# Kernel tuning notes

Hardware: AMD Instinct MI355X
Metric: run time of the kernel (lower is better)

## Reference

```python
import jax, jax.numpy as jnp
import numpy as np

N_SUP, N_SUB, LATENT, OUT = 256, 1024, 512, 200


def list_of_distances(X, Y):
    # squared Euclidean pairwise distances: (len(X), len(Y))
    xx = jnp.sum(X * X, axis=1, keepdims=True)          # (n, 1)
    yy = jnp.sum(Y * Y, axis=1)[None, :]                # (1, m)
    return xx - 2.0 * (X @ Y.T) + yy


def setup_inputs() -> dict:
    key = jax.random.key(0)
    ks = jax.random.split(key, 7)
    x = jax.random.normal(ks[0], (32768, LATENT), dtype=jnp.float32)
    sup_prototypes = jax.random.uniform(ks[1], (N_SUP, LATENT), dtype=jnp.float32)
    sub_prototypes = jax.random.uniform(ks[2], (N_SUB, LATENT), dtype=jnp.float32)
    lim1 = 1.0 / np.sqrt(N_SUP)
    lim2 = 1.0 / np.sqrt(N_SUB)
    W1 = jax.random.uniform(ks[3], (OUT, N_SUP), dtype=jnp.float32, minval=-lim1, maxval=lim1)
    b1 = jax.random.uniform(ks[4], (OUT,), dtype=jnp.float32, minval=-lim1, maxval=lim1)
    W2 = jax.random.uniform(ks[5], (OUT, N_SUB), dtype=jnp.float32, minval=-lim2, maxval=lim2)
    b2 = jax.random.uniform(ks[6], (OUT,), dtype=jnp.float32, minval=-lim2, maxval=lim2)
    return {"x": x, "sup_prototypes": sup_prototypes, "sub_prototypes": sub_prototypes,
            "W1": W1, "b1": b1, "W2": W2, "b2": b2}


def reference(x, sup_prototypes, sub_prototypes, W1, b1, W2, b2):
    sup_input_dist = list_of_distances(x, sup_prototypes)   # (B, n_sup)
    sub_input_dist = list_of_distances(x, sub_prototypes)   # (B, n_sub)
    sup_out = sup_input_dist @ W1.T + b1                     # (B, out)
    sub_out = sub_input_dist @ W2.T + b2                     # (B, out)
    sub_clones = jax.lax.stop_gradient(sub_prototypes)
    super_sub_dist = list_of_distances(sup_prototypes, sub_clones)  # (n_sup, n_sub)
    r1 = jnp.mean(jnp.min(sub_input_dist, axis=0))
    r2 = jnp.mean(jnp.min(sub_input_dist, axis=1))
    r3 = jnp.mean(jnp.min(super_sub_dist, axis=1))
    r4 = jnp.mean(jnp.min(super_sub_dist, axis=0))
    return (sub_out, sup_out, r1, r2, r3, r4)
```

## Files before the change

kernel.cpp:

```cpp
#include <hip/hip_runtime.h>
#include <stdint.h>

#define BATCH   32768
#define NSUP    256
#define NSUB    1024
#define LATENT  512
#define NOUT    200
#define SUP_OFF ((size_t)BATCH * NOUT)

typedef unsigned short u16;
typedef __attribute__((ext_vector_type(8))) __bf16 bf16x8;
typedef __attribute__((ext_vector_type(4))) float  floatx4;

typedef const __attribute__((address_space(1))) void* gptr_t;
typedef __attribute__((address_space(3))) void* sptr_t;

__device__ __forceinline__ void gload16(const void* g, void* l) {
  __builtin_amdgcn_global_load_lds((gptr_t)g, (sptr_t)l, 16, 0, 0);
}

__device__ __forceinline__ floatx4 mfma_bf16(bf16x8 a, bf16x8 b, floatx4 c) {
  return __builtin_amdgcn_mfma_f32_16x16x32_bf16(a, b, c, 0, 0, 0);
}

__device__ __forceinline__ u16 f2bf(float f) {
  unsigned int u = __float_as_uint(f);
  u += 0x7FFFu + ((u >> 16) & 1u);
  return (u16)(u >> 16);
}

__device__ __forceinline__ size_t bfoff(int c, int k) {
  return (size_t)(c >> 4) * 8192 + (size_t)((k >> 5) * 512)
       + (size_t)((((k >> 3) & 3) * 16 + (c & 15)) * 8) + (size_t)(k & 7);
}

__global__ __launch_bounds__(256) void k_setup(const float* __restrict__ sup,
    const float* __restrict__ sub, const float* __restrict__ W1,
    const float* __restrict__ W2, u16* __restrict__ sups, u16* __restrict__ subs,
    u16* __restrict__ Bf, float* __restrict__ MtF, float* __restrict__ xxsup,
    float* __restrict__ yys, unsigned int* __restrict__ minbuf,
    float* __restrict__ out4) {
  __shared__ float lw[8 * 256];
  int bx = blockIdx.x;
  if (bx >= 458) {
    int idx = bx - 458;
    if (idx >= 400) {
      int z = idx - 400;
      int k = (z & 1) * 256 + threadIdx.x;
      int o0 = 400 + (z >> 1) * 8;
      for (int oo = 0; oo < 8; oo++) Bf[bfoff(o0 + oo, k)] = 0;
      return;
    }
    int jc = idx & 3;
    int kb = (idx >> 2) & 1;
    int o0 = (idx >> 3) * 8;
    int k  = kb * 256 + threadIdx.x;
    const float* P; const float* W; int n, ow;
    if (o0 < 200) { P = sup; W = W1; n = NSUP;  ow = o0; }
    else          { P = sub; W = W2; n = NSUB;  ow = o0 - 200; }
    int nq = n >> 2;
    int j0 = jc * nq;
    for (int i = threadIdx.x; i < 8 * nq; i += 256) {
      int oo = i / nq, j = i - oo * nq;
      lw[oo * 256 + j] = W[(size_t)(ow + oo) * n + j0 + j];
    }
    __syncthreads();
    float a[8] = {};
    for (int j = 0; j < nq; j += 8) {
      float pv[8];
#pragma unroll
      for (int u = 0; u < 8; u++) pv[u] = P[(size_t)(j0 + j + u) * LATENT + k];
#pragma unroll
      for (int oo = 0; oo < 8; oo++) {
        float acc = 0.f;
#pragma unroll
        for (int u = 0; u < 8; u++) acc += pv[u] * lw[oo * 256 + j + u];
        a[oo] += acc;
      }
    }
#pragma unroll
    for (int oo = 0; oo < 8; oo++)
      MtF[((size_t)jc * 400 + o0 + oo) * 512 + k] = a[oo];
    return;
  }
  if (bx >= 320) {
    if (bx == 457) { if (threadIdx.x < 4) out4[threadIdx.x] = 0.f; return; }
    int i = (bx - 320) * 256 + threadIdx.x;
    if (i < BATCH + NSUP + 2 * NSUB) minbuf[i] = 0x7F800000u;
    return;
  }
  int row  = bx * 4 + (threadIdx.x >> 6);
  int lane = threadIdx.x & 63;
  const float* src; u16* dst; float* nrm; int subrow = -1;
  if (row < NSUP) { src = sup + (size_t)row * LATENT; dst = sups + (size_t)row * LATENT; nrm = xxsup + row; }
  else { int r = row - NSUP; subrow = r; src = sub + (size_t)r * LATENT; dst = subs + (size_t)r * LATENT; nrm = yys + r; }
  const float* s = src + lane * 8;
  float4 v0 = ((const float4*)s)[0];
  float4 v1 = ((const float4*)s)[1];
  float ss = v0.x*v0.x + v0.y*v0.y + v0.z*v0.z + v0.w*v0.w
           + v1.x*v1.x + v1.y*v1.y + v1.z*v1.z + v1.w*v1.w;
  uint4 o;
  o.x = (unsigned)f2bf(v0.x) | ((unsigned)f2bf(v0.y) << 16);
  o.y = (unsigned)f2bf(v0.z) | ((unsigned)f2bf(v0.w) << 16);
  o.z = (unsigned)f2bf(v1.x) | ((unsigned)f2bf(v1.y) << 16);
  o.w = (unsigned)f2bf(v1.z) | ((unsigned)f2bf(v1.w) << 16);
  *((uint4*)(dst + lane * 8)) = o;
  if (subrow >= 0) {
    size_t off = (size_t)(32 + (subrow >> 4)) * 8192 + (size_t)((lane >> 2) * 512)
               + (size_t)((((lane & 3) * 16) + (subrow & 15)) * 8);
    *((uint4*)(Bf + off)) = o;
  }
  for (int off = 32; off; off >>= 1) ss += __shfl_down(ss, off);
  if (lane == 0) *nrm = ss;
}

__global__ __launch_bounds__(256) void k_scc(const float* __restrict__ W1,
    const float* __restrict__ b1, const float* __restrict__ W2,
    const float* __restrict__ b2, const float* __restrict__ xxsup,
    const float* __restrict__ yys, float* __restrict__ sc, float* __restrict__ cc,
    const u16* __restrict__ sups, const u16* __restrict__ subs,
    const float* __restrict__ MtF, u16* __restrict__ Bf,
    unsigned int* __restrict__ rowmin, unsigned int* __restrict__ colsup) {
  __shared__ __align__(16) u16 lA[128 * 64];
  __shared__ __align__(16) u16 lB[128 * 64];
  int bx = blockIdx.x;
  if (bx >= 116) {
    int o = bx - 116;
    for (int k = threadIdx.x; k < 512; k += 256) {
      float s = MtF[((size_t)0 * 400 + o) * 512 + k]
              + MtF[((size_t)1 * 400 + o) * 512 + k]
              + MtF[((size_t)2 * 400 + o) * 512 + k]
              + MtF[((size_t)3 * 400 + o) * 512 + k];
      Bf[bfoff(o, k)] = f2bf(-2.f * s);
    }
    return;
  }
  if (bx >= 100) {
    int bid = bx - 100;
    int cb = bid & 7;
    size_t arow0 = (size_t)(bid >> 3) * 128;
    const u16* B = subs + (size_t)cb * 128 * LATENT;
    floatx4 acc[4][4] = {};
    int t = threadIdx.x, wave = t >> 6, lane = t & 63;
    int l16 = lane & 15, qq = lane >> 4;
    int wm = (wave >> 1) * 64, wn = (wave & 1) * 64;
    int sq = (lane & 7) ^ (lane >> 3);
    const u16* Ab = sups + arow0 * LATENT;
    int soff[4]; u16 *dA[4], *dB[4];
#pragma unroll
    for (int i = 0; i < 4; i++) {
      int s = i * 256 + t;
      soff[i] = (s >> 3) * LATENT + sq * 8;
      int sbase = (i * 256 + wave * 64) * 8;
      dA[i] = lA + sbase; dB[i] = lB + sbase;
    }
    for (int k0 = 0; k0 < LATENT; k0 += 64) {
#pragma unroll
      for (int i = 0; i < 4; i++) gload16(Ab + soff[i] + k0, dA[i]);
#pragma unroll
      for (int i = 0; i < 4; i++) gload16(B  + soff[i] + k0, dB[i]);
      __syncthreads();
#pragma unroll
      for (int ks = 0; ks < 2; ks++) {
        bf16x8 af[4], bvv[4];
        int sw = ((ks * 4 + qq) ^ (l16 & 7)) * 8;
#pragma unroll
        for (int f = 0; f < 4; f++) {
          af[f]  = *(const bf16x8*)(lA + (wm + f * 16 + l16) * 64 + sw);
          bvv[f] = *(const bf16x8*)(lB + (wn + f * 16 + l16) * 64 + sw);
        }
#pragma unroll
        for (int fm = 0; fm < 4; fm++)
#pragma unroll
          for (int fn = 0; fn < 4; fn++)
            acc[fm][fn] = mfma_bf16(af[fm], bvv[fn], acc[fm][fn]);
      }
      __syncthreads();
    }
    int colb = cb * 128 + wn + l16;
    float yv[4];
#pragma unroll
    for (int fn = 0; fn < 4; fn++) yv[fn] = yys[colb + fn * 16];
    float cmin[4] = {3.4e38f, 3.4e38f, 3.4e38f, 3.4e38f};
#pragma unroll
    for (int fm = 0; fm < 4; fm++) {
#pragma unroll
      for (int r = 0; r < 4; r++) {
        int row = (int)arow0 + wm + fm * 16 + qq * 4 + r;
        float xvv = xxsup[row];
        float rmin = 3.4e38f;
#pragma unroll
        for (int fn = 0; fn < 4; fn++) {
          float d = xvv - 2.0f * acc[fm][fn][r] + yv[fn];
          rmin = fminf(rmin, d);
          cmin[fn] = fminf(cmin[fn], d);
        }
        for (int off = 1; off < 16; off <<= 1) rmin = fminf(rmin, __shfl_xor(rmin, off));
        if (l16 == 0) atomicMin(rowmin + BATCH + row, __float_as_uint(rmin));
      }
    }
#pragma unroll
    for (int fn = 0; fn < 4; fn++) {
      float v = cmin[fn];
      v = fminf(v, __shfl_xor(v, 16));
      v = fminf(v, __shfl_xor(v, 32));
      if (qq == 0) atomicMin(colsup + colb + fn * 16, __float_as_uint(v));
    }
    return;
  }
  int wave = threadIdx.x >> 6, lane = threadIdx.x & 63;
  int o = bx * 4 + wave;
  if (o >= 400) return;
  int n; const float* Wr; const float* yy;
  if (o < 200) { n = NSUP; Wr = W1 + (size_t)o * NSUP; yy = xxsup; }
  else         { n = NSUB; Wr = W2 + (size_t)(o - 200) * NSUB; yy = yys; }
  float s = 0.f, c = 0.f;
  for (int j = lane; j < n; j += 64) { float w = Wr[j]; s += w; c += w * yy[j]; }
  for (int off = 32; off; off >>= 1) { s += __shfl_down(s, off); c += __shfl_down(c, off); }
  if (lane == 0) { sc[o] = s; cc[o] = c + ((o < 200) ? b1[o] : b2[o - 200]); }
}

__global__ __launch_bounds__(512, 2) void k_gemm_x(const float* __restrict__ x,
    const u16* __restrict__ Bf, const float* __restrict__ yys,
    const float* __restrict__ sc, const float* __restrict__ cc,
    float* __restrict__ out, unsigned int* __restrict__ rowmin,
    unsigned int* __restrict__ colx) {
  __shared__ __align__(16) u16 lA[128 * 512];
  __shared__ float lxx[128];
  int t = threadIdx.x, wave = t >> 6, lane = t & 63;
  int l16 = lane & 15, qq = lane >> 4;
  int wr = wave >> 2, wc = wave & 3;
  size_t arow0 = (size_t)blockIdx.x * 128;

  const float* Ab = x + arow0 * LATENT;
#pragma unroll
  for (int i = 0; i < 16; i++) {
    int row = i * 8 + wave;
    const float* s = Ab + (size_t)row * LATENT + lane * 8;
    float4 v0 = ((const float4*)s)[0];
    float4 v1 = ((const float4*)s)[1];
    float ss = v0.x*v0.x + v0.y*v0.y + v0.z*v0.z + v0.w*v0.w
             + v1.x*v1.x + v1.y*v1.y + v1.z*v1.z + v1.w*v1.w;
    uint4 o;
    o.x = (unsigned)f2bf(v0.x) | ((unsigned)f2bf(v0.y) << 16);
    o.y = (unsigned)f2bf(v0.z) | ((unsigned)f2bf(v0.w) << 16);
    o.z = (unsigned)f2bf(v1.x) | ((unsigned)f2bf(v1.y) << 16);
    o.w = (unsigned)f2bf(v1.z) | ((unsigned)f2bf(v1.w) << 16);
    *((uint4*)(lA + ((row * 64) + (lane ^ (row & 7))) * 8)) = o;
    for (int off = 32; off; off >>= 1) ss += __shfl_down(ss, off);
    if (lane == 0) lxx[row] = ss;
  }
  __syncthreads();

  float xv[4][4];
#pragma unroll
  for (int mf = 0; mf < 4; mf++)
#pragma unroll
    for (int r = 0; r < 4; r++) xv[mf][r] = lxx[wr * 64 + mf * 16 + qq * 4 + r];
  float rmreg[4][4];
#pragma unroll
  for (int mf = 0; mf < 4; mf++)
#pragma unroll
    for (int r = 0; r < 4; r++) rmreg[mf][r] = 3.4e38f;

#pragma unroll 1
  for (int p = 0; p < 6; p++) {
    floatx4 acc[4][4] = {};
    const u16* Bw = Bf + (size_t)(p * 16 + wc * 4) * 8192 + lane * 8;
#pragma unroll 2
    for (int k0 = 0; k0 < LATENT; k0 += 64) {
      bf16x8 bv[4][2];
#pragma unroll
      for (int nf = 0; nf < 4; nf++)
#pragma unroll
        for (int ks = 0; ks < 2; ks++)
          bv[nf][ks] = *(const bf16x8*)(Bw + nf * 8192 + k0 * 16 + ks * 512);
#pragma unroll
      for (int ks = 0; ks < 2; ks++) {
        bf16x8 a[4];
#pragma unroll
        for (int mf = 0; mf < 4; mf++) {
          int row = wr * 64 + mf * 16 + l16;
          int kc = (k0 >> 3) + ks * 4 + qq;
          a[mf] = *(const bf16x8*)(lA + ((row * 64) + (kc ^ (row & 7))) * 8);
        }
#pragma unroll
        for (int mf = 0; mf < 4; mf++)
#pragma unroll
          for (int nf = 0; nf < 4; nf++)
            acc[mf][nf] = mfma_bf16(a[mf], bv[nf][ks], acc[mf][nf]);
      }
    }
    if (p < 2) {
      int colbase = p * 256 + wc * 64;
#pragma unroll
      for (int nf = 0; nf < 4; nf++) {
        int c = colbase + nf * 16 + l16;
        if (c < 400) {
          float scv = sc[c], ccv = cc[c];
#pragma unroll
          for (int mf = 0; mf < 4; mf++)
#pragma unroll
            for (int r = 0; r < 4; r++) {
              size_t row = arow0 + wr * 64 + mf * 16 + qq * 4 + r;
              float v = acc[mf][nf][r] + xv[mf][r] * scv + ccv;
              size_t idx = (c < 200) ? (SUP_OFF + row * NOUT + c)
                                     : (row * NOUT + (c - 200));
              out[idx] = v;
            }
        }
      }
    } else {
      int colbase = p * 256 + wc * 64 - 512;
#pragma unroll
      for (int nf = 0; nf < 4; nf++) {
        int cs = colbase + nf * 16 + l16;
        float yv = yys[cs];
        float cmin = 3.4e38f;
#pragma unroll
        for (int mf = 0; mf < 4; mf++)
#pragma unroll
          for (int r = 0; r < 4; r++) {
            float d = xv[mf][r] - 2.0f * acc[mf][nf][r] + yv;
            rmreg[mf][r] = fminf(rmreg[mf][r], d);
            cmin = fminf(cmin, d);
          }
        cmin = fminf(cmin, __shfl_xor(cmin, 16));
        cmin = fminf(cmin, __shfl_xor(cmin, 32));
        if (qq == 0) atomicMin(colx + cs, __float_as_uint(cmin));
      }
    }
  }
#pragma unroll
  for (int mf = 0; mf < 4; mf++)
#pragma unroll
    for (int r = 0; r < 4; r++) {
      float v = rmreg[mf][r];
      v = fminf(v, __shfl_xor(v, 1));
      v = fminf(v, __shfl_xor(v, 2));
      v = fminf(v, __shfl_xor(v, 4));
      v = fminf(v, __shfl_xor(v, 8));
      if (l16 == 0)
        atomicMin(rowmin + arow0 + wr * 64 + mf * 16 + qq * 4 + r, __float_as_uint(v));
    }
}

__global__ __launch_bounds__(256) void k_final2(const unsigned int* __restrict__ rowmin,
    const unsigned int* __restrict__ colx, const unsigned int* __restrict__ colsup,
    float* __restrict__ out4) {
  int bx = blockIdx.x, t = threadIdx.x;
  const unsigned int* src; int n; float scale; int slot;
  if (bx < 32)      { src = rowmin + bx * 1024; n = 1024; scale = 1.f / BATCH; slot = 1; }
  else if (bx == 32){ src = colx;               n = 1024; scale = 1.f / NSUB;  slot = 0; }
  else if (bx == 33){ src = rowmin + BATCH;     n = 256;  scale = 1.f / NSUP;  slot = 2; }
  else              { src = colsup;             n = 1024; scale = 1.f / NSUB;  slot = 3; }
  float s = 0.f;
  for (int i = t; i < n; i += 256) s += __uint_as_float(src[i]);
  __shared__ float red[4];
  for (int off = 32; off; off >>= 1) s += __shfl_down(s, off);
  if ((t & 63) == 0) red[t >> 6] = s;
  __syncthreads();
  if (t == 0) atomicAdd(out4 + slot, (red[0] + red[1] + red[2] + red[3]) * scale);
}

extern "C" void kernel_launch(void* const* d_in, const int* in_sizes, int n_in,
                              void* d_out, int out_size, void* d_ws, size_t ws_size,
                              hipStream_t stream) {
  const float* x   = (const float*)d_in[0];
  const float* sup = (const float*)d_in[1];
  const float* sub = (const float*)d_in[2];
  const float* W1  = (const float*)d_in[3];
  const float* b1  = (const float*)d_in[4];
  const float* W2  = (const float*)d_in[5];
  const float* b2  = (const float*)d_in[6];
  float* out = (float*)d_out;

  char* p = (char*)d_ws;
  u16* Bf    = (u16*)p;            p += (size_t)(512 + NSUB) * LATENT * 2;
  u16* subs  = (u16*)p;            p += (size_t)NSUB * LATENT * 2;
  u16* sups  = (u16*)p;            p += (size_t)NSUP * LATENT * 2;
  float* xxsup = (float*)p;        p += NSUP * 4;
  float* yys   = (float*)p;        p += NSUB * 4;
  float* sc    = (float*)p;        p += 512 * 4;
  float* cc    = (float*)p;        p += 512 * 4;
  unsigned int* rowmin = (unsigned int*)p; p += (size_t)(BATCH + NSUP) * 4;
  unsigned int* colx   = (unsigned int*)p; p += (size_t)NSUB * 4;
  unsigned int* colsup = (unsigned int*)p; p += (size_t)NSUB * 4;
  float* MtF   = (float*)p;        p += (size_t)4 * 400 * 512 * 4;

  float* out4 = out + 2 * SUP_OFF;

  hipLaunchKernelGGL(k_setup, dim3(886), dim3(256), 0, stream,
                     sup, sub, W1, W2, sups, subs, Bf, MtF, xxsup, yys, rowmin, out4);
  hipLaunchKernelGGL(k_scc, dim3(516), dim3(256), 0, stream,
                     W1, b1, W2, b2, xxsup, yys, sc, cc, sups, subs, MtF, Bf,
                     rowmin, colsup);
  hipLaunchKernelGGL(k_gemm_x, dim3(BATCH / 128), dim3(512), 0, stream,
                     x, Bf, yys, sc, cc, out, rowmin, colx);
  hipLaunchKernelGGL(k_final2, dim3(35), dim3(256), 0, stream, rowmin, colx, colsup, out4);
}
```

Before: 118.6 us.

## Shrink gemm row tile to 64 and spread eight waves across columns

The main GEMM kernel now processes 64 rows per block instead of 128, with all eight waves splitting the columns (512 per pass, 3 passes) rather than a 2x4 row/column wave grid over 6 passes. LDS use is halved and launch bounds raised to 4 blocks per CU, aiming for more occupancy and more blocks across the device. Row-min reduction now happens per pass with extra atomics, and each B fragment is reused across fewer A rows, so global/L2 traffic for B per output increases.

```diff
diff --git a/kernel.cpp b/kernel.cpp
--- a/kernel.cpp
+++ b/kernel.cpp
@@ -220,21 +220,21 @@
   if (lane == 0) { sc[o] = s; cc[o] = c + ((o < 200) ? b1[o] : b2[o - 200]); }
 }
 
-__global__ __launch_bounds__(512, 2) void k_gemm_x(const float* __restrict__ x,
+__global__ __launch_bounds__(512, 4) void k_gemm_x(const float* __restrict__ x,
     const u16* __restrict__ Bf, const float* __restrict__ yys,
     const float* __restrict__ sc, const float* __restrict__ cc,
     float* __restrict__ out, unsigned int* __restrict__ rowmin,
     unsigned int* __restrict__ colx) {
-  __shared__ __align__(16) u16 lA[128 * 512];
-  __shared__ float lxx[128];
+  __shared__ __align__(16) u16 lA[64 * 512];
+  __shared__ float lxx[64];
   int t = threadIdx.x, wave = t >> 6, lane = t & 63;
   int l16 = lane & 15, qq = lane >> 4;
-  int wr = wave >> 2, wc = wave & 3;
-  size_t arow0 = (size_t)blockIdx.x * 128;
+  int wc = wave;
+  size_t arow0 = (size_t)blockIdx.x * 64;
 
   const float* Ab = x + arow0 * LATENT;
 #pragma unroll
-  for (int i = 0; i < 16; i++) {
+  for (int i = 0; i < 8; i++) {
     int row = i * 8 + wave;
     const float* s = Ab + (size_t)row * LATENT + lane * 8;
     float4 v0 = ((const float4*)s)[0];
@@ -252,21 +252,10 @@
   }
   __syncthreads();
 
-  float xv[4][4];
-#pragma unroll
-  for (int mf = 0; mf < 4; mf++)
-#pragma unroll
-    for (int r = 0; r < 4; r++) xv[mf][r] = lxx[wr * 64 + mf * 16 + qq * 4 + r];
-  float rmreg[4][4];
-#pragma unroll
-  for (int mf = 0; mf < 4; mf++)
-#pragma unroll
-    for (int r = 0; r < 4; r++) rmreg[mf][r] = 3.4e38f;
-
 #pragma unroll 1
-  for (int p = 0; p < 6; p++) {
+  for (int p = 0; p < 3; p++) {
     floatx4 acc[4][4] = {};
-    const u16* Bw = Bf + (size_t)(p * 16 + wc * 4) * 8192 + lane * 8;
+    const u16* Bw = Bf + (size_t)(p * 32 + wc * 4) * 8192 + lane * 8;
 #pragma unroll 2
     for (int k0 = 0; k0 < LATENT; k0 += 64) {
       bf16x8 bv[4][2];
@@ -280,7 +269,7 @@
         bf16x8 a[4];
 #pragma unroll
         for (int mf = 0; mf < 4; mf++) {
-          int row = wr * 64 + mf * 16 + l16;
+          int row = mf * 16 + l16;
           int kc = (k0 >> 3) + ks * 4 + qq;
           a[mf] = *(const bf16x8*)(lA + ((row * 64) + (kc ^ (row & 7))) * 8);
         }
@@ -291,8 +280,13 @@
             acc[mf][nf] = mfma_bf16(a[mf], bv[nf][ks], acc[mf][nf]);
       }
     }
-    if (p < 2) {
-      int colbase = p * 256 + wc * 64;
+    float xr[4][4];
+#pragma unroll
+    for (int mf = 0; mf < 4; mf++)
+#pragma unroll
+      for (int r = 0; r < 4; r++) xr[mf][r] = lxx[mf * 16 + qq * 4 + r];
+    if (p == 0) {
+      int colbase = wc * 64;
 #pragma unroll
       for (int nf = 0; nf < 4; nf++) {
         int c = colbase + nf * 16 + l16;
@@ -302,8 +296,8 @@
           for (int mf = 0; mf < 4; mf++)
 #pragma unroll
             for (int r = 0; r < 4; r++) {
-              size_t row = arow0 + wr * 64 + mf * 16 + qq * 4 + r;
-              float v = acc[mf][nf][r] + xv[mf][r] * scv + ccv;
+              size_t row = arow0 + mf * 16 + qq * 4 + r;
+              float v = acc[mf][nf][r] + xr[mf][r] * scv + ccv;
               size_t idx = (c < 200) ? (SUP_OFF + row * NOUT + c)
                                      : (row * NOUT + (c - 200));
               out[idx] = v;
@@ -311,7 +305,12 @@
         }
       }
     } else {
-      int colbase = p * 256 + wc * 64 - 512;
+      int colbase = (p - 1) * 512 + wc * 64;
+      float rm[4][4];
+#pragma unroll
+      for (int mf = 0; mf < 4; mf++)
+#pragma unroll
+        for (int r = 0; r < 4; r++) rm[mf][r] = 3.4e38f;
 #pragma unroll
       for (int nf = 0; nf < 4; nf++) {
         int cs = colbase + nf * 16 + l16;
@@ -321,28 +320,28 @@
         for (int mf = 0; mf < 4; mf++)
 #pragma unroll
           for (int r = 0; r < 4; r++) {
-            float d = xv[mf][r] - 2.0f * acc[mf][nf][r] + yv;
-            rmreg[mf][r] = fminf(rmreg[mf][r], d);
+            float d = xr[mf][r] - 2.0f * acc[mf][nf][r] + yv;
+            rm[mf][r] = fminf(rm[mf][r], d);
             cmin = fminf(cmin, d);
           }
         cmin = fminf(cmin, __shfl_xor(cmin, 16));
         cmin = fminf(cmin, __shfl_xor(cmin, 32));
         if (qq == 0) atomicMin(colx + cs, __float_as_uint(cmin));
       }
-    }
-  }
-#pragma unroll
-  for (int mf = 0; mf < 4; mf++)
-#pragma unroll
-    for (int r = 0; r < 4; r++) {
-      float v = rmreg[mf][r];
-      v = fminf(v, __shfl_xor(v, 1));
-      v = fminf(v, __shfl_xor(v, 2));
-      v = fminf(v, __shfl_xor(v, 4));
-      v = fminf(v, __shfl_xor(v, 8));
-      if (l16 == 0)
-        atomicMin(rowmin + arow0 + wr * 64 + mf * 16 + qq * 4 + r, __float_as_uint(v));
-    }
+#pragma unroll
+      for (int mf = 0; mf < 4; mf++)
+#pragma unroll
+        for (int r = 0; r < 4; r++) {
+          float v = rm[mf][r];
+          v = fminf(v, __shfl_xor(v, 1));
+          v = fminf(v, __shfl_xor(v, 2));
+          v = fminf(v, __shfl_xor(v, 4));
+          v = fminf(v, __shfl_xor(v, 8));
+          if (l16 == 0)
+            atomicMin(rowmin + arow0 + mf * 16 + qq * 4 + r, __float_as_uint(v));
+        }
+    }
+  }
 }
 
 __global__ __launch_bounds__(256) void k_final2(const unsigned int* __restrict__ rowmin,
@@ -395,7 +394,7 @@
   hipLaunchKernelGGL(k_scc, dim3(516), dim3(256), 0, stream,
                      W1, b1, W2, b2, xxsup, yys, sc, cc, sups, subs, MtF, Bf,
                      rowmin, colsup);
-  hipLaunchKernelGGL(k_gemm_x, dim3(BATCH / 128), dim3(512), 0, stream,
+  hipLaunchKernelGGL(k_gemm_x, dim3(BATCH / 64), dim3(512), 0, stream,
                      x, Bf, yys, sc, cc, out, rowmin, colx);
   hipLaunchKernelGGL(k_final2, dim3(35), dim3(256), 0, stream, rowmin, colx, colsup, out4);
 }
```

Result: slower. 227.3 us (+91.6%).
